# Performance work log

Hardware: AMD Instinct MI355X
Metric: run time of the kernel (lower is better)

Reference implementation:

```python
import jax, jax.numpy as jnp
import numpy as np
import math

EMBED_DIM = 1024
NUM_HEADS = 16
B, T = 4, 2048
HEAD_DIM = EMBED_DIM // NUM_HEADS


def setup_inputs() -> dict:
    key = jax.random.key(0)
    ks = jax.random.split(key, 9)
    s = 1.0 / math.sqrt(EMBED_DIM)
    x = jax.random.normal(ks[0], (B, T, EMBED_DIM), dtype=jnp.float32)
    # causal mask, broadcastable over (B, H)
    mask = jnp.tril(jnp.ones((T, T), dtype=bool))[None, None, :, :]
    Wq = jax.random.normal(ks[1], (EMBED_DIM, EMBED_DIM), dtype=jnp.float32) * s
    bq = jnp.zeros((EMBED_DIM,), dtype=jnp.float32)
    Wk = jax.random.normal(ks[2], (EMBED_DIM, EMBED_DIM), dtype=jnp.float32) * s
    bk = jnp.zeros((EMBED_DIM,), dtype=jnp.float32)
    Wv = jax.random.normal(ks[3], (EMBED_DIM, EMBED_DIM), dtype=jnp.float32) * s
    bv = jnp.zeros((EMBED_DIM,), dtype=jnp.float32)
    Wo = jax.random.normal(ks[4], (EMBED_DIM, EMBED_DIM), dtype=jnp.float32) * s
    bo = jnp.zeros((EMBED_DIM,), dtype=jnp.float32)
    return {"x": x, "mask": mask, "Wq": Wq, "bq": bq, "Wk": Wk, "bk": bk,
            "Wv": Wv, "bv": bv, "Wo": Wo, "bo": bo}


def reference(x, mask, Wq, bq, Wk, bk, Wv, bv, Wo, bo):
    Bsz, Tlen, C = x.shape
    H, D = NUM_HEADS, HEAD_DIM
    q = (x @ Wq + bq).reshape(Bsz, Tlen, H, D).transpose(0, 2, 1, 3)  # [B,H,T,D]
    k = (x @ Wk + bk).reshape(Bsz, Tlen, H, D).transpose(0, 2, 1, 3)
    v = (x @ Wv + bv).reshape(Bsz, Tlen, H, D).transpose(0, 2, 1, 3)
    scores = jnp.einsum('bhtd,bhsd->bhts', q, k) / math.sqrt(D)  # [B,H,T,T]
    scores = jnp.where(mask, scores, jnp.float32(-1e9))
    attn = jax.nn.softmax(scores, axis=-1)
    out = jnp.einsum('bhts,bhsd->bhtd', attn, v)  # [B,H,T,D]
    out = out.transpose(0, 2, 1, 3).reshape(Bsz, Tlen, C)
    return out @ Wo + bo
```

## Files before the change

kernel.cpp:

```cpp
#include <hip/hip_runtime.h>

#define SEQ   2048
#define NH    16
#define HD    64
#define EMB   1024
#define NB    4
#define MTOT  (NB*SEQ)
#define NT    (SEQ/64)

typedef _Float16 f16;
typedef _Float16 f16x4 __attribute__((ext_vector_type(4)));
typedef _Float16 f16x8 __attribute__((ext_vector_type(8)));
typedef float    f32x4 __attribute__((ext_vector_type(4)));

#define MFMA_F16(a,b,c) __builtin_amdgcn_mfma_f32_16x16x32_f16(a,b,c,0,0,0)

#define QSCALE 0.18033688011112043f

__device__ __forceinline__ float fast_exp2(float x) {
#if __has_builtin(__builtin_amdgcn_exp2f)
  return __builtin_amdgcn_exp2f(x);
#else
  return exp2f(x);
#endif
}

__device__ __forceinline__ void gload16(const f16* g, f16* l) {
  __builtin_amdgcn_global_load_lds(
      (const __attribute__((address_space(1))) void*)g,
      (__attribute__((address_space(3))) void*)l, 16, 0, 0);
}

__global__ __launch_bounds__(256) void prep_kernel(
    const float* __restrict__ x, f16* __restrict__ xh,
    const float* __restrict__ W0, const float* __restrict__ W1,
    const float* __restrict__ W2, const float* __restrict__ W3,
    f16* __restrict__ O0, f16* __restrict__ O1,
    f16* __restrict__ O2, f16* __restrict__ O3) {
  const int z = blockIdx.z;
  if (z < 4) {
    const float* W = (z==0)?W0:(z==1)?W1:(z==2)?W2:W3;
    f16* O        = (z==0)?O0:(z==1)?O1:(z==2)?O2:O3;
    __shared__ float Tl[64][68];
    const int t = threadIdx.x;
    const int k0 = blockIdx.x * 64, n0 = blockIdx.y * 64;
    {
      const int r = t >> 2, c0 = (t & 3) * 16;
      const float* src = W + (size_t)(k0 + r) * EMB + n0 + c0;
      #pragma unroll
      for (int j = 0; j < 4; ++j) {
        float4 v = *(const float4*)(src + 4 * j);
        Tl[c0+4*j+0][r]=v.x; Tl[c0+4*j+1][r]=v.y;
        Tl[c0+4*j+2][r]=v.z; Tl[c0+4*j+3][r]=v.w;
      }
    }
    __syncthreads();
    {
      const int n = t >> 2, c0 = (t & 3) * 16;
      f16* dst = O + (size_t)(n0 + n) * EMB + k0 + c0;
      #pragma unroll
      for (int j = 0; j < 2; ++j) {
        f16x8 o;
        #pragma unroll
        for (int u = 0; u < 8; ++u) o[u] = (f16)Tl[n][c0 + 8*j + u];
        *(f16x8*)(dst + 8 * j) = o;
      }
    }
  } else {
    const int blk = (z - 4) * 256 + blockIdx.y * 16 + blockIdx.x;
    #pragma unroll
    for (int it = 0; it < 8; ++it) {
      size_t i = (((size_t)blk * 8 + it) * 256 + threadIdx.x) * 8;
      float4 a = *(const float4*)(x + i);
      float4 b = *(const float4*)(x + i + 4);
      f16x8 o;
      o[0]=(f16)a.x; o[1]=(f16)a.y; o[2]=(f16)a.z; o[3]=(f16)a.w;
      o[4]=(f16)b.x; o[5]=(f16)b.y; o[6]=(f16)b.z; o[7]=(f16)b.w;
      *(f16x8*)(xh + i) = o;
    }
  }
}

template<int MODE>
__device__ __forceinline__ void gemm_core(
    const f16* __restrict__ A, const f16* __restrict__ Bt,
    const float* __restrict__ bias, void* __restrict__ out,
    int m0, int n0, float scale) {
  __shared__ f16 As[128 * 64];
  __shared__ f16 Bs[128 * 64];
  const int tid  = threadIdx.x;
  const int lane = tid & 63, w = tid >> 6;
  const int g = lane >> 4, lx = lane & 15;
  const int wr = w >> 1, wc = w & 1;
  const int sr = lane >> 3, sc = lane & 7;

  f32x4 acc[4][4];
  const f32x4 z4 = {0.f, 0.f, 0.f, 0.f};
  #pragma unroll
  for (int i = 0; i < 4; ++i)
    #pragma unroll
    for (int j = 0; j < 4; ++j) acc[i][j] = z4;

  for (int k0 = 0; k0 < EMB; k0 += 64) {
    __syncthreads();
    #pragma unroll
    for (int ci = 0; ci < 4; ++ci) {
      const int i = 4 * w + ci;
      const int r = i * 8 + sr;
      const int c = sc ^ (r & 7);
      gload16(A  + (size_t)(m0 + r) * EMB + k0 + c * 8, &As[i * 512]);
      gload16(Bt + (size_t)(n0 + r) * EMB + k0 + c * 8, &Bs[i * 512]);
    }
    __syncthreads();

    #pragma unroll
    for (int h = 0; h < 2; ++h) {
      f16x8 af[4], bf[4];
      #pragma unroll
      for (int mf = 0; mf < 4; ++mf) {
        const int row = wr * 64 + mf * 16 + lx;
        const int off = (row * 128 + h * 64 + g * 16) ^ ((row & 7) << 4);
        af[mf] = *(const f16x8*)((const char*)As + off);
      }
      #pragma unroll
      for (int nf = 0; nf < 4; ++nf) {
        const int row = wc * 64 + nf * 16 + lx;
        const int off = (row * 128 + h * 64 + g * 16) ^ ((row & 7) << 4);
        bf[nf] = *(const f16x8*)((const char*)Bs + off);
      }
      #pragma unroll
      for (int mf = 0; mf < 4; ++mf)
        #pragma unroll
        for (int nf = 0; nf < 4; ++nf)
          acc[mf][nf] = MFMA_F16(af[mf], bf[nf], acc[mf][nf]);
    }
  }

  #pragma unroll
  for (int mf = 0; mf < 4; ++mf) {
    #pragma unroll
    for (int nf = 0; nf < 4; ++nf) {
      const int n  = n0 + wc * 64 + nf * 16 + lx;
      const int mb = m0 + wr * 64 + mf * 16 + g * 4;
      const float bv = bias[n];
      if (MODE == 2) {
        float* op = (float*)out;
        #pragma unroll
        for (int r = 0; r < 4; ++r)
          op[(size_t)(mb + r) * EMB + n] = acc[mf][nf][r] + bv;
      } else {
        const int b = mb >> 11, tt = mb & (SEQ - 1);
        const int hh = n >> 6, d = n & (HD - 1);
        f16* op = (f16*)out;
        if (MODE == 0) {
          #pragma unroll
          for (int r = 0; r < 4; ++r)
            op[((size_t)(b * NH + hh) * SEQ + tt + r) * HD + d] =
                (f16)((acc[mf][nf][r] + bv) * scale);
        } else {
          f16x4 o;
          #pragma unroll
          for (int r = 0; r < 4; ++r) o[r] = (f16)(acc[mf][nf][r] + bv);
          *(f16x4*)(op + ((size_t)(b * NH + hh) * HD + d) * SEQ + tt) = o;
        }
      }
    }
  }
}

__global__ __launch_bounds__(256) void qkv_gemm_kernel(
    const f16* __restrict__ xh, const f16* __restrict__ wqt,
    const f16* __restrict__ wkt, const f16* __restrict__ wvt,
    const float* __restrict__ bq, const float* __restrict__ bk,
    const float* __restrict__ bv,
    f16* __restrict__ qh, f16* __restrict__ kh, f16* __restrict__ vth) {
  const int z = blockIdx.z;
  const int m0 = blockIdx.x * 128, n0 = blockIdx.y * 128;
  if (z == 0)      gemm_core<0>(xh, wqt, bq, qh, m0, n0, QSCALE);
  else if (z == 1) gemm_core<0>(xh, wkt, bk, kh, m0, n0, 1.0f);
  else             gemm_core<1>(xh, wvt, bv, vth, m0, n0, 1.0f);
}

__global__ __launch_bounds__(256) void proj_gemm_kernel(
    const f16* __restrict__ ath, const f16* __restrict__ wot,
    const float* __restrict__ bo, float* __restrict__ out) {
  gemm_core<2>(ath, wot, bo, out, blockIdx.x * 128, blockIdx.y * 128, 1.0f);
}

__global__ __launch_bounds__(256, 4) void attn_kernel(
    const f16* __restrict__ Qh, const f16* __restrict__ Kh,
    const f16* __restrict__ Vth, f16* __restrict__ Opart,
    float* __restrict__ mPart, float* __restrict__ lPart) {
  __shared__ f16 Ks[64 * 64];
  __shared__ f16 Vs[64 * 64];
  __shared__ f16 Ps[4][16 * 64];
  const int tid  = threadIdx.x;
  const int lane = tid & 63, w = tid >> 6;
  const int g = lane >> 4, lx = lane & 15;
  const int sr = lane >> 3, sc = lane & 7;
  const int bid = blockIdx.x;
  const int xcd   = bid & 7;
  const int idx   = bid >> 3;
  const int split = idx & 1;
  const int p     = (idx >> 1) & 15;
  const int bh    = xcd + 8 * (idx >> 5);
  const int qlo = p, qhi = NT - 1 - p;
  const int nkt = qhi + 1;
  const f16* qp = Qh  + (size_t)bh * SEQ * HD;
  const f16* kp = Kh  + (size_t)bh * SEQ * HD;
  const f16* vp = Vth + (size_t)bh * HD * SEQ;
  const int row0[2] = {qlo * 64 + w * 16, qhi * 64 + w * 16};

  f16x8 qf[2][2];
  #pragma unroll
  for (int part = 0; part < 2; ++part) {
    const int qrow = row0[part] + lx;
    #pragma unroll
    for (int h = 0; h < 2; ++h)
      qf[part][h] = *(const f16x8*)(qp + (size_t)qrow * HD + h * 32 + g * 8);
  }

  const f32x4 z4 = {0.f, 0.f, 0.f, 0.f};
  f32x4 oa[2][4];
  float m_i[2] = {-1e30f, -1e30f}, l_i[2] = {0.f, 0.f};
  #pragma unroll
  for (int part = 0; part < 2; ++part)
    #pragma unroll
    for (int df = 0; df < 4; ++df) oa[part][df] = z4;

  for (int kt = split; kt < nkt; kt += 2) {
    __syncthreads();
    #pragma unroll
    for (int ci = 0; ci < 2; ++ci) {
      const int i = 2 * w + ci;
      const int r = i * 8 + sr;
      const int c = sc ^ (r & 7);
      gload16(kp + (size_t)(kt * 64 + r) * HD + c * 8, &Ks[i * 512]);
      gload16(vp + (size_t)r * SEQ + kt * 64 + c * 8,  &Vs[i * 512]);
    }
    __syncthreads();

    const int npart = (kt <= qlo) ? 2 : 1;
    #pragma unroll
    for (int pi = 0; pi < 2; ++pi) {
      if (pi >= npart) continue;
      const int part = 1 - pi;
      const int qrow = row0[part] + lx;
      const bool diag = (kt == (part ? qhi : qlo));

      f32x4 sa[4];
      #pragma unroll
      for (int sf = 0; sf < 4; ++sf) sa[sf] = z4;
      __builtin_amdgcn_s_setprio(1);
      #pragma unroll
      for (int h = 0; h < 2; ++h)
        #pragma unroll
        for (int sf = 0; sf < 4; ++sf) {
          const int row = sf * 16 + lx;
          const int off = (row * 128 + h * 64 + g * 16) ^ ((row & 7) << 4);
          f16x8 kf = *(const f16x8*)((const char*)Ks + off);
          sa[sf] = MFMA_F16(kf, qf[part][h], sa[sf]);
        }
      __builtin_amdgcn_s_setprio(0);

      float rmax = -1e30f;
      #pragma unroll
      for (int sf = 0; sf < 4; ++sf)
        #pragma unroll
        for (int r = 0; r < 4; ++r) {
          float vsc = sa[sf][r];
          if (diag) {
            const int kv = kt * 64 + sf * 16 + g * 4 + r;
            if (kv > qrow) vsc = -1e30f;
          }
          sa[sf][r] = vsc;
          rmax = fmaxf(rmax, vsc);
        }
      rmax = fmaxf(rmax, __shfl_xor(rmax, 16));
      rmax = fmaxf(rmax, __shfl_xor(rmax, 32));
      const float mnew = fmaxf(m_i[part], rmax);
      const float corr = fast_exp2(m_i[part] - mnew);
      m_i[part] = mnew;
      float rsum = 0.f;
      #pragma unroll
      for (int sf = 0; sf < 4; ++sf)
        #pragma unroll
        for (int r = 0; r < 4; ++r) {
          const float pv = fast_exp2(sa[sf][r] - mnew);
          sa[sf][r] = pv;
          rsum += pv;
        }
      rsum += __shfl_xor(rsum, 16);
      rsum += __shfl_xor(rsum, 32);
      l_i[part] = l_i[part] * corr + rsum;

      #pragma unroll
      for (int sf = 0; sf < 4; ++sf) {
        f16x4 p4;
        #pragma unroll
        for (int r = 0; r < 4; ++r) p4[r] = (f16)sa[sf][r];
        const int off = (lx * 128 + sf * 32 + g * 8) ^ ((lx & 7) << 4);
        *(f16x4*)((char*)Ps[w] + off) = p4;
      }

      #pragma unroll
      for (int r = 0; r < 4; ++r) {
        const float cr = __shfl(corr, g * 4 + r, 64);
        #pragma unroll
        for (int df = 0; df < 4; ++df) oa[part][df][r] *= cr;
      }

      __builtin_amdgcn_s_setprio(1);
      #pragma unroll
      for (int hk = 0; hk < 2; ++hk) {
        const int offp = (lx * 128 + hk * 64 + g * 16) ^ ((lx & 7) << 4);
        f16x8 pf = *(const f16x8*)((const char*)Ps[w] + offp);
        #pragma unroll
        for (int df = 0; df < 4; ++df) {
          const int row = df * 16 + lx;
          const int offv = (row * 128 + hk * 64 + g * 16) ^ ((row & 7) << 4);
          f16x8 vf = *(const f16x8*)((const char*)Vs + offv);
          oa[part][df] = MFMA_F16(pf, vf, oa[part][df]);
        }
      }
      __builtin_amdgcn_s_setprio(0);
    }
  }

  const size_t sb = (size_t)split * 64 + bh;
  #pragma unroll
  for (int part = 0; part < 2; ++part) {
    if (lane < 16) {
      mPart[sb * SEQ + row0[part] + lane] = m_i[part];
      lPart[sb * SEQ + row0[part] + lane] = l_i[part];
    }
    #pragma unroll
    for (int r = 0; r < 4; ++r) {
      const int t = row0[part] + g * 4 + r;
      f16* dst = Opart + ((size_t)sb * SEQ + t) * HD;
      #pragma unroll
      for (int df = 0; df < 4; ++df)
        dst[df * 16 + lx] = (f16)(oa[part][df][r]);
    }
  }
}

__global__ __launch_bounds__(256) void combine_kernel(
    const f16* __restrict__ Opart, const float* __restrict__ mPart,
    const float* __restrict__ lPart, f16* __restrict__ Att) {
  const int G = blockIdx.x * 256 + threadIdx.x;
  const int chunk = G & 7;
  const int rowid = G >> 3;
  const int bh = rowid >> 11, t = rowid & (SEQ - 1);
  const int b = bh >> 4, h = bh & 15;
  const size_t i1 = (size_t)bh * SEQ + t;
  const size_t i2 = (size_t)(64 + bh) * SEQ + t;
  const float m1 = mPart[i1], m2 = mPart[i2];
  const float l1 = lPart[i1], l2 = lPart[i2];
  const float mx = fmaxf(m1, m2);
  const float w1 = fast_exp2(m1 - mx), w2 = fast_exp2(m2 - mx);
  const float inv = 1.f / (l1 * w1 + l2 * w2);
  const f16x8 o1 = *(const f16x8*)(Opart + i1 * HD + chunk * 8);
  const f16x8 o2 = *(const f16x8*)(Opart + i2 * HD + chunk * 8);
  f16x8 o;
  #pragma unroll
  for (int j = 0; j < 8; ++j)
    o[j] = (f16)(((float)o1[j] * w1 + (float)o2[j] * w2) * inv);
  *(f16x8*)(Att + ((size_t)b * SEQ + t) * EMB + h * HD + chunk * 8) = o;
}

extern "C" void kernel_launch(void* const* d_in, const int* in_sizes, int n_in,
                              void* d_out, int out_size, void* d_ws, size_t ws_size,
                              hipStream_t stream) {
  (void)in_sizes; (void)n_in; (void)out_size; (void)ws_size;
  const float* x  = (const float*)d_in[0];
  const float* Wq = (const float*)d_in[2];
  const float* bq = (const float*)d_in[3];
  const float* Wk = (const float*)d_in[4];
  const float* bk = (const float*)d_in[5];
  const float* Wv = (const float*)d_in[6];
  const float* bv = (const float*)d_in[7];
  const float* Wo = (const float*)d_in[8];
  const float* bo = (const float*)d_in[9];

  f16* xh    = (f16*)d_ws;
  f16* wqt   = xh  + (size_t)MTOT * EMB;
  f16* wkt   = wqt + (size_t)EMB * EMB;
  f16* wvt   = wkt + (size_t)EMB * EMB;
  f16* wot   = wvt + (size_t)EMB * EMB;
  f16* qh    = wot + (size_t)EMB * EMB;
  f16* kh    = qh  + (size_t)MTOT * EMB;
  f16* vth   = kh  + (size_t)MTOT * EMB;
  f16* ath   = vth + (size_t)MTOT * EMB;
  f16* Opart = ath + (size_t)MTOT * EMB;
  float* mP  = (float*)(Opart + (size_t)2 * 64 * SEQ * HD);
  float* lP  = mP + (size_t)2 * 64 * SEQ;

  prep_kernel<<<dim3(16, 16, 6), 256, 0, stream>>>(
      x, xh, Wq, Wk, Wv, Wo, wqt, wkt, wvt, wot);
  qkv_gemm_kernel<<<dim3(MTOT / 128, EMB / 128, 3), 256, 0, stream>>>(
      xh, wqt, wkt, wvt, bq, bk, bv, qh, kh, vth);
  attn_kernel<<<dim3((NT / 2) * 2 * NB * NH), 256, 0, stream>>>(
      qh, kh, vth, Opart, mP, lP);
  combine_kernel<<<dim3(NB * NH * SEQ * 8 / 256), 256, 0, stream>>>(
      Opart, mP, lP, ath);
  proj_gemm_kernel<<<dim3(MTOT / 128, EMB / 128), 256, 0, stream>>>(
      ath, wot, bo, (float*)d_out);
}
```

Before: 191.6 us.

## Fuse split-KV combine into attention kernel via last-block atomic flag

Removes the separate combine kernel. Each attention block now fences, atomically increments a per-(q-tile pair, head) counter, and the second of the two split blocks to finish merges both partials into the final attention output. This saves one kernel launch and its scheduling gap, and the combine reads likely hit in cache. In exchange it adds a memset launch, thread fences, and a serial tail of combine work on the last-finishing blocks.

```diff
diff --git a/kernel.cpp b/kernel.cpp
--- a/kernel.cpp
+++ b/kernel.cpp
@@ -190,7 +190,8 @@
 __global__ __launch_bounds__(256, 4) void attn_kernel(
     const f16* __restrict__ Qh, const f16* __restrict__ Kh,
     const f16* __restrict__ Vth, f16* __restrict__ Opart,
-    float* __restrict__ mPart, float* __restrict__ lPart) {
+    float* __restrict__ mPart, float* __restrict__ lPart,
+    f16* __restrict__ Att, int* __restrict__ flags) {
   __shared__ f16 Ks[64 * 64];
   __shared__ f16 Vs[64 * 64];
   __shared__ f16 Ps[4][16 * 64];
@@ -343,30 +344,37 @@
         dst[df * 16 + lx] = (f16)(oa[part][df][r]);
     }
   }
-}
-
-__global__ __launch_bounds__(256) void combine_kernel(
-    const f16* __restrict__ Opart, const float* __restrict__ mPart,
-    const float* __restrict__ lPart, f16* __restrict__ Att) {
-  const int G = blockIdx.x * 256 + threadIdx.x;
-  const int chunk = G & 7;
-  const int rowid = G >> 3;
-  const int bh = rowid >> 11, t = rowid & (SEQ - 1);
-  const int b = bh >> 4, h = bh & 15;
-  const size_t i1 = (size_t)bh * SEQ + t;
-  const size_t i2 = (size_t)(64 + bh) * SEQ + t;
-  const float m1 = mPart[i1], m2 = mPart[i2];
-  const float l1 = lPart[i1], l2 = lPart[i2];
-  const float mx = fmaxf(m1, m2);
-  const float w1 = fast_exp2(m1 - mx), w2 = fast_exp2(m2 - mx);
-  const float inv = 1.f / (l1 * w1 + l2 * w2);
-  const f16x8 o1 = *(const f16x8*)(Opart + i1 * HD + chunk * 8);
-  const f16x8 o2 = *(const f16x8*)(Opart + i2 * HD + chunk * 8);
-  f16x8 o;
-  #pragma unroll
-  for (int j = 0; j < 8; ++j)
-    o[j] = (f16)(((float)o1[j] * w1 + (float)o2[j] * w2) * inv);
-  *(f16x8*)(Att + ((size_t)b * SEQ + t) * EMB + h * HD + chunk * 8) = o;
+
+  __threadfence();
+  __shared__ int lastFlag;
+  if (tid == 0)
+    lastFlag = (atomicAdd(&flags[p * 64 + bh], 1) == 1);
+  __syncthreads();
+  if (lastFlag) {
+    __threadfence();
+    const int b = bh >> 4, hh = bh & 15;
+    #pragma unroll
+    for (int it = 0; it < 4; ++it) {
+      const int unit  = it * 256 + tid;
+      const int chunk = unit & 7;
+      const int ridx  = unit >> 3;
+      const int t = (ridx < 64) ? (qlo * 64 + ridx) : (qhi * 64 + ridx - 64);
+      const size_t i1 = (size_t)bh * SEQ + t;
+      const size_t i2 = (size_t)(64 + bh) * SEQ + t;
+      const float m1 = mPart[i1], m2 = mPart[i2];
+      const float l1 = lPart[i1], l2 = lPart[i2];
+      const float mx = fmaxf(m1, m2);
+      const float w1 = fast_exp2(m1 - mx), w2 = fast_exp2(m2 - mx);
+      const float inv = 1.f / (l1 * w1 + l2 * w2);
+      const f16x8 o1 = *(const f16x8*)(Opart + i1 * HD + chunk * 8);
+      const f16x8 o2 = *(const f16x8*)(Opart + i2 * HD + chunk * 8);
+      f16x8 o;
+      #pragma unroll
+      for (int j = 0; j < 8; ++j)
+        o[j] = (f16)(((float)o1[j] * w1 + (float)o2[j] * w2) * inv);
+      *(f16x8*)(Att + ((size_t)b * SEQ + t) * EMB + hh * HD + chunk * 8) = o;
+    }
+  }
 }
 
 extern "C" void kernel_launch(void* const* d_in, const int* in_sizes, int n_in,
@@ -395,15 +403,15 @@
   f16* Opart = ath + (size_t)MTOT * EMB;
   float* mP  = (float*)(Opart + (size_t)2 * 64 * SEQ * HD);
   float* lP  = mP + (size_t)2 * 64 * SEQ;
-
+  int* flags = (int*)(lP + (size_t)2 * 64 * SEQ);
+
+  hipMemsetAsync(flags, 0, 1024 * sizeof(int), stream);
   prep_kernel<<<dim3(16, 16, 6), 256, 0, stream>>>(
       x, xh, Wq, Wk, Wv, Wo, wqt, wkt, wvt, wot);
   qkv_gemm_kernel<<<dim3(MTOT / 128, EMB / 128, 3), 256, 0, stream>>>(
       xh, wqt, wkt, wvt, bq, bk, bv, qh, kh, vth);
   attn_kernel<<<dim3((NT / 2) * 2 * NB * NH), 256, 0, stream>>>(
-      qh, kh, vth, Opart, mP, lP);
-  combine_kernel<<<dim3(NB * NH * SEQ * 8 / 256), 256, 0, stream>>>(
-      Opart, mP, lP, ath);
+      qh, kh, vth, Opart, mP, lP, ath, flags);
   proj_gemm_kernel<<<dim3(MTOT / 128, EMB / 128), 256, 0, stream>>>(
       ath, wot, bo, (float*)d_out);
 }
```

After: 572.3 us. +198.6%, slower.
